# Performance work log

Measured on AMD Instinct MI355X. Metric: run time of the kernel, lower is better.

Reference implementation:

```python
import jax, jax.numpy as jnp
import numpy as np

N_HEAD = 16

def setup_inputs() -> dict:
    key = jax.random.key(0)
    k1, k2, k3 = jax.random.split(key, 3)
    B, T, C = 4, 2048, 1024
    x = jax.random.normal(k1, (B, T, C), dtype=jnp.float32)
    W_attn = jax.random.normal(k2, (C, 3 * C), dtype=jnp.float32) * (1.0 / np.sqrt(C))
    b_attn = jnp.zeros((3 * C,), dtype=jnp.float32)
    W_proj = jax.random.normal(k3, (C, C), dtype=jnp.float32) * (1.0 / np.sqrt(C))
    b_proj = jnp.zeros((C,), dtype=jnp.float32)
    return {"x": x, "W_attn": W_attn, "b_attn": b_attn, "W_proj": W_proj, "b_proj": b_proj, "train": 0}

def reference(x, W_attn, b_attn, W_proj, b_proj, train):
    # Causal self-attention, eval mode (dropout = identity since dropout=0.0 / train=False).
    B, T, C = x.shape
    H = N_HEAD
    hd = C // H
    qkv = x @ W_attn + b_attn                      # [B, T, 3C]
    q, k, v = jnp.split(qkv, 3, axis=-1)
    def to_heads(a):
        return a.reshape(B, T, H, hd).swapaxes(1, 2)   # [B, H, T, hd]
    q, k, v = to_heads(q), to_heads(k), to_heads(v)
    scale = 1.0 / jnp.sqrt(jnp.asarray(hd, dtype=x.dtype))
    attn = jnp.einsum('bhqd,bhkd->bhqk', q, k) * scale   # [B, H, T, T]
    causal = jnp.tril(jnp.ones((T, T), dtype=bool))
    attn = jnp.where(causal, attn, -jnp.inf)
    p = jax.nn.softmax(attn, axis=-1)
    y = jnp.einsum('bhqk,bhkd->bhqd', p, v)              # [B, H, T, hd]
    y = y.swapaxes(1, 2).reshape(B, T, C)
    return y @ W_proj + b_proj
```

## Files before the change

kernel.cpp:

```cpp
#include <hip/hip_runtime.h>
#include <hip/hip_bf16.h>
#include <math.h>

typedef __attribute__((ext_vector_type(8))) short short8;
typedef __attribute__((ext_vector_type(4))) short short4v;
typedef __attribute__((ext_vector_type(4))) float floatx4;
using bf16 = __hip_bfloat16;

#define DEVI __device__ __forceinline__

DEVI floatx4 fzero4() { floatx4 z; z[0]=0.f; z[1]=0.f; z[2]=0.f; z[3]=0.f; return z; }

DEVI float ex2(float x) {
  float r;
  asm("v_exp_f32 %0, %1" : "=v"(r) : "v"(x));
  return r;
}

DEVI unsigned short f2b(float x) {
  union { bf16 h; unsigned short u; } c;
  c.h = __float2bfloat16(x);
  return c.u;
}

DEVI floatx4 mfma16(short4v a, short4v b, floatx4 c) {
#if __has_builtin(__builtin_amdgcn_mfma_f32_16x16x16bf16_1k)
  return __builtin_amdgcn_mfma_f32_16x16x16bf16_1k(a, b, c, 0, 0, 0);
#else
  floatx4 d;
  asm("v_mfma_f32_16x16x16_bf16 %0, %1, %2, %3" : "=v"(d) : "v"(a), "v"(b), "v"(c));
  return d;
#endif
}

DEVI void gload16(const bf16* g, bf16* l) {
  typedef __attribute__((address_space(1))) const void gv_t;
  typedef __attribute__((address_space(3))) void lv_t;
  __builtin_amdgcn_global_load_lds((gv_t*)g, (lv_t*)l, 16, 0, 0);
}

__global__ __launch_bounds__(256) void k_cast(const float* __restrict__ in,
                                              bf16* __restrict__ out, int n) {
  int i = (blockIdx.x * 256 + threadIdx.x) * 8;
  if (i >= n) return;
  float4 a = *(const float4*)(in + i);
  float4 b = *(const float4*)(in + i + 4);
  short8 v;
  v[0] = (short)f2b(a.x); v[1] = (short)f2b(a.y);
  v[2] = (short)f2b(a.z); v[3] = (short)f2b(a.w);
  v[4] = (short)f2b(b.x); v[5] = (short)f2b(b.y);
  v[6] = (short)f2b(b.z); v[7] = (short)f2b(b.w);
  *(short8*)(out + i) = v;
}

__global__ __launch_bounds__(256) void k_transpose(const float* __restrict__ in,
                                                   bf16* __restrict__ out,
                                                   int R, int C) {
  __shared__ float tile[32][33];
  int x = blockIdx.x * 32 + threadIdx.x;
  for (int i = threadIdx.y; i < 32; i += 8) {
    int y = blockIdx.y * 32 + i;
    tile[i][threadIdx.x] = (y < R && x < C) ? in[(size_t)y * C + x] : 0.f;
  }
  __syncthreads();
  int ox = blockIdx.y * 32 + threadIdx.x;
  for (int i = threadIdx.y; i < 32; i += 8) {
    int oy = blockIdx.x * 32 + i;
    if (oy < C && ox < R) out[(size_t)oy * R + ox] = __float2bfloat16(tile[threadIdx.x][i]);
  }
}

template<int MODE>
__global__ __launch_bounds__(256) void k_gemm(
    const bf16* __restrict__ A, const bf16* __restrict__ Bt,
    const float* __restrict__ bias,
    bf16* __restrict__ Qo, bf16* __restrict__ Ko, bf16* __restrict__ Vo,
    float* __restrict__ Fo, int M, int N, int Kd) {
  __shared__ bf16 sA[128 * 32];
  __shared__ bf16 sB[128 * 32];
  const int tid = threadIdx.x;
  const int w = tid >> 6, l = tid & 63;
  const int lg = l >> 4, li = l & 15;
  const int wr = w >> 1, wc = w & 1;
  const int m0 = blockIdx.y * 128, n0 = blockIdx.x * 128;

  const int r0 = tid >> 2, ko0 = (tid & 3) * 8;
  const bf16* pa0 = A + (size_t)(m0 + r0) * Kd + ko0;
  const bf16* pa1 = A + (size_t)(m0 + 64 + r0) * Kd + ko0;
  const bf16* pb0 = Bt + (size_t)(n0 + r0) * Kd + ko0;
  const bf16* pb1 = Bt + (size_t)(n0 + 64 + r0) * Kd + ko0;

  floatx4 acc[4][4];
#pragma unroll
  for (int i = 0; i < 4; ++i)
#pragma unroll
    for (int j = 0; j < 4; ++j) acc[i][j] = fzero4();

  for (int k0 = 0; k0 < Kd; k0 += 32) {
    __syncthreads();
    gload16(pa0 + k0, sA + w * 512);
    gload16(pa1 + k0, sA + 2048 + w * 512);
    gload16(pb0 + k0, sB + w * 512);
    gload16(pb1 + k0, sB + 2048 + w * 512);
    __syncthreads();
    short8 af[4], bfr[4];
#pragma unroll
    for (int i = 0; i < 4; ++i)
      af[i] = *(const short8*)&sA[(wr * 64 + i * 16 + li) * 32 + lg * 8];
#pragma unroll
    for (int j = 0; j < 4; ++j)
      bfr[j] = *(const short8*)&sB[(wc * 64 + j * 16 + li) * 32 + lg * 8];
#pragma unroll
    for (int i = 0; i < 4; ++i)
#pragma unroll
      for (int j = 0; j < 4; ++j)
        acc[i][j] = __builtin_amdgcn_mfma_f32_16x16x32_bf16(af[i], bfr[j], acc[i][j], 0, 0, 0);
  }

#pragma unroll
  for (int i = 0; i < 4; ++i) {
#pragma unroll
    for (int j = 0; j < 4; ++j) {
      const int ng = n0 + wc * 64 + j * 16 + li;
      const float bs = bias[ng];
#pragma unroll
      for (int r = 0; r < 4; ++r) {
        const int mg = m0 + wr * 64 + i * 16 + lg * 4 + r;
        const float v = acc[i][j][r] + bs;
        if (MODE == 0) {
          const int bb = mg >> 11, t = mg & 2047;
          const int d = ng & 63;
          if (ng < 1024) {
            const int h = ng >> 6;
            Qo[(((size_t)bb * 16 + h) * 2048 + t) * 64 + d] = __float2bfloat16(v * 0.18033688011112042f);
          } else if (ng < 2048) {
            const int h = (ng - 1024) >> 6;
            Ko[(((size_t)bb * 16 + h) * 2048 + t) * 64 + d] = __float2bfloat16(v);
          } else {
            const int h = (ng - 2048) >> 6;
            Vo[(((size_t)bb * 16 + h) * 64 + d) * 2048 + t] = __float2bfloat16(v);
          }
        } else {
          Fo[(size_t)mg * N + ng] = v;
        }
      }
    }
  }
}

#define T_SEQ 2048

__global__ __launch_bounds__(256) void k_attn(
    const bf16* __restrict__ Q, const bf16* __restrict__ K,
    const bf16* __restrict__ Vt, bf16* __restrict__ Y) {
  __shared__ bf16 sK[2][64 * 64];
  __shared__ bf16 sV[2][64 * 64];

  const int tid = threadIdx.x;
  const int w = tid >> 6, l = tid & 63;
  const int lg = l >> 4, li = l & 15;
  const int bid = blockIdx.x;
  const int s = bid >> 3;
  const int bh = (bid & 7) * 8 + (s & 7);
  const int tb = 15 - (s >> 3);
  const int b = bh >> 4, h = bh & 15;

  const bf16* Qp = Q + (size_t)bh * (T_SEQ * 64);
  const bf16* Kp = K + (size_t)bh * (T_SEQ * 64);
  const bf16* Vp = Vt + (size_t)bh * (64 * T_SEQ);

  const int q0 = tb * 128;
  const int wq0 = q0 + w * 32;
  const int nst = (q0 + 128) >> 6;

  short8 aq[2][2];
#pragma unroll
  for (int rg = 0; rg < 2; ++rg)
#pragma unroll
    for (int dc = 0; dc < 2; ++dc)
      aq[rg][dc] = *(const short8*)(Qp + (size_t)(wq0 + rg * 16 + li) * 64 + dc * 32 + lg * 8);

  floatx4 o[2][4];
#pragma unroll
  for (int rg = 0; rg < 2; ++rg)
#pragma unroll
    for (int f = 0; f < 4; ++f) o[rg][f] = fzero4();
  float m[2] = {-INFINITY, -INFINITY};
  float lsum[2] = {0.f, 0.f};

  auto STAGE = [&](int buf, int k0) {
#pragma unroll
    for (int half = 0; half < 2; ++half) {
      const int c = half * 256 + tid;
      const int row = c >> 3, cs = c & 7;
      const int sc = cs ^ (row & 7);
      bf16* kb = &sK[buf][(half * 256 + w * 64) * 8];
      bf16* vb = &sV[buf][(half * 256 + w * 64) * 8];
      gload16(Kp + (size_t)(k0 + row) * 64 + sc * 8, kb);
      gload16(Vp + (size_t)row * T_SEQ + k0 + sc * 8, vb);
    }
  };

  int cur = 0;
  STAGE(0, 0);
  __syncthreads();
  for (int t = 0; t < nst; ++t) {
    const int k0 = t << 6;
    if (t + 1 < nst) STAGE(cur ^ 1, k0 + 64);
    if (k0 <= wq0 + 31) {
      floatx4 s[2][4];
#pragma unroll
      for (int kt = 0; kt < 4; ++kt) {
        const int rowk = kt * 16 + li;
        const short8 kb0 = *(const short8*)&sK[cur][rowk * 64 + ((lg ^ (rowk & 7)) * 8)];
        const short8 kb1 = *(const short8*)&sK[cur][rowk * 64 + (((4 + lg) ^ (rowk & 7)) * 8)];
#pragma unroll
        for (int rg = 0; rg < 2; ++rg) {
          floatx4 acc = __builtin_amdgcn_mfma_f32_16x16x32_bf16(kb0, aq[rg][0], fzero4(), 0, 0, 0);
          s[rg][kt] = __builtin_amdgcn_mfma_f32_16x16x32_bf16(kb1, aq[rg][1], acc, 0, 0, 0);
        }
      }
      if (k0 + 63 > wq0) {
#pragma unroll
        for (int rg = 0; rg < 2; ++rg) {
          const int qg = wq0 + rg * 16 + li;
#pragma unroll
          for (int kt = 0; kt < 4; ++kt) {
            const int kgb = k0 + kt * 16 + lg * 4;
#pragma unroll
            for (int r = 0; r < 4; ++r)
              if (kgb + r > qg) s[rg][kt][r] = -1e30f;
          }
        }
      }
      float pm[2];
#pragma unroll
      for (int rg = 0; rg < 2; ++rg) {
        float m0_ = fmaxf(fmaxf(s[rg][0][0], s[rg][0][1]), fmaxf(s[rg][0][2], s[rg][0][3]));
        float m1_ = fmaxf(fmaxf(s[rg][1][0], s[rg][1][1]), fmaxf(s[rg][1][2], s[rg][1][3]));
        float m2_ = fmaxf(fmaxf(s[rg][2][0], s[rg][2][1]), fmaxf(s[rg][2][2], s[rg][2][3]));
        float m3_ = fmaxf(fmaxf(s[rg][3][0], s[rg][3][1]), fmaxf(s[rg][3][2], s[rg][3][3]));
        float p = fmaxf(fmaxf(m0_, m1_), fmaxf(m2_, m3_));
        p = fmaxf(p, __shfl_xor(p, 16));
        p = fmaxf(p, __shfl_xor(p, 32));
        pm[rg] = p;
      }
      const float need = fmaxf(pm[0] - m[0], pm[1] - m[1]);
      if (!__all(need <= 8.0f)) {
#pragma unroll
        for (int rg = 0; rg < 2; ++rg) {
          const float mn = fmaxf(m[rg], pm[rg]);
          const float a = ex2(m[rg] - mn);
          m[rg] = mn;
          lsum[rg] *= a;
          float ar[4];
#pragma unroll
          for (int r = 0; r < 4; ++r) ar[r] = __shfl(a, lg * 4 + r);
#pragma unroll
          for (int f = 0; f < 4; ++f) {
            o[rg][f][0] *= ar[0]; o[rg][f][1] *= ar[1];
            o[rg][f][2] *= ar[2]; o[rg][f][3] *= ar[3];
          }
        }
      }
      short4v pa4[2][4];
#pragma unroll
      for (int rg = 0; rg < 2; ++rg) {
#pragma unroll
        for (int kt = 0; kt < 4; ++kt) {
          const float e0 = ex2(s[rg][kt][0] - m[rg]);
          const float e1 = ex2(s[rg][kt][1] - m[rg]);
          const float e2 = ex2(s[rg][kt][2] - m[rg]);
          const float e3 = ex2(s[rg][kt][3] - m[rg]);
          lsum[rg] += (e0 + e1) + (e2 + e3);
          short4v pv;
          pv[0] = (short)f2b(e0); pv[1] = (short)f2b(e1);
          pv[2] = (short)f2b(e2); pv[3] = (short)f2b(e3);
          pa4[rg][kt] = pv;
        }
      }
#pragma unroll
      for (int f = 0; f < 4; ++f) {
        const int rowv = f * 16 + li;
        const int rx = rowv & 7;
#pragma unroll
        for (int kt = 0; kt < 4; ++kt) {
          const int cc = 2 * kt + (lg >> 1);
          const short4v vb4 = *(const short4v*)&sV[cur][rowv * 64 + (((cc ^ rx) << 3) | ((lg & 1) << 2))];
          o[0][f] = mfma16(pa4[0][kt], vb4, o[0][f]);
          o[1][f] = mfma16(pa4[1][kt], vb4, o[1][f]);
        }
      }
    }
    __syncthreads();
    cur ^= 1;
  }
#pragma unroll
  for (int rg = 0; rg < 2; ++rg) {
    float Ls = lsum[rg];
    Ls += __shfl_xor(Ls, 16);
    Ls += __shfl_xor(Ls, 32);
#pragma unroll
    for (int r = 0; r < 4; ++r) {
      const float inv = 1.0f / __shfl(Ls, lg * 4 + r);
      const int qg = wq0 + rg * 16 + lg * 4 + r;
      const size_t base = ((size_t)b * T_SEQ + qg) * 1024 + h * 64;
#pragma unroll
      for (int f = 0; f < 4; ++f)
        Y[base + f * 16 + li] = __float2bfloat16(o[rg][f][r] * inv);
    }
  }
}

extern "C" void kernel_launch(void* const* d_in, const int* in_sizes, int n_in,
                              void* d_out, int out_size, void* d_ws, size_t ws_size,
                              hipStream_t stream) {
  const float* x      = (const float*)d_in[0];
  const float* W_attn = (const float*)d_in[1];
  const float* b_attn = (const float*)d_in[2];
  const float* W_proj = (const float*)d_in[3];
  const float* b_proj = (const float*)d_in[4];
  float* out = (float*)d_out;

  char* ws = (char*)d_ws;
  bf16* Wt_a = (bf16*)(ws);
  bf16* Wt_p = (bf16*)(ws + 6291456);
  bf16* Qb   = (bf16*)(ws + 8388608);
  bf16* Kb   = (bf16*)(ws + 25165824);
  bf16* Vtb  = (bf16*)(ws + 41943040);
  bf16* x_bf = (bf16*)(ws + 58720256);
  bf16* Yb   = x_bf;

  k_cast<<<4096, 256, 0, stream>>>(x, x_bf, 8388608);
  k_transpose<<<dim3(96, 32), dim3(32, 8), 0, stream>>>(W_attn, Wt_a, 1024, 3072);
  k_transpose<<<dim3(32, 32), dim3(32, 8), 0, stream>>>(W_proj, Wt_p, 1024, 1024);
  k_gemm<0><<<dim3(24, 64), 256, 0, stream>>>(x_bf, Wt_a, b_attn, Qb, Kb, Vtb,
                                              nullptr, 8192, 3072, 1024);
  k_attn<<<1024, 256, 0, stream>>>(Qb, Kb, Vtb, Yb);
  k_gemm<1><<<dim3(8, 64), 256, 0, stream>>>(Yb, Wt_p, b_proj, nullptr, nullptr,
                                             nullptr, out, 8192, 1024, 1024);
}
```

Measured before the change: 222.1 us.

## Double-buffer GEMM LDS tiles and remap blocks for XCD-local L2 reuse

Converts the GEMM k-loop to a two-stage LDS double buffer, issuing the next tile's global-to-LDS loads before computing the current one and waiting with vmcnt counts instead of full syncthreads. It also flattens the grid and remaps block indices so blocks dispatched to the same XCD work on neighbouring M rows, to improve L2 hit rates. The cost is doubled LDS per block, which could reduce occupancy, plus reliance on hand-written waitcnt correctness.

```diff
diff --git a/kernel.cpp b/kernel.cpp
--- a/kernel.cpp
+++ b/kernel.cpp
@@ -76,13 +76,15 @@
     const float* __restrict__ bias,
     bf16* __restrict__ Qo, bf16* __restrict__ Ko, bf16* __restrict__ Vo,
     float* __restrict__ Fo, int M, int N, int Kd) {
-  __shared__ bf16 sA[128 * 32];
-  __shared__ bf16 sB[128 * 32];
+  __shared__ bf16 sA[2][128 * 32];
+  __shared__ bf16 sB[2][128 * 32];
   const int tid = threadIdx.x;
   const int w = tid >> 6, l = tid & 63;
   const int lg = l >> 4, li = l & 15;
   const int wr = w >> 1, wc = w & 1;
-  const int m0 = blockIdx.y * 128, n0 = blockIdx.x * 128;
+  const int ii = blockIdx.x >> 3, xcd = blockIdx.x & 7;
+  const int bx = ii >> 3, by = xcd * 8 + (ii & 7);
+  const int m0 = by * 128, n0 = bx * 128;
 
   const int r0 = tid >> 2, ko0 = (tid & 3) * 8;
   const bf16* pa0 = A + (size_t)(m0 + r0) * Kd + ko0;
@@ -96,25 +98,37 @@
 #pragma unroll
     for (int j = 0; j < 4; ++j) acc[i][j] = fzero4();
 
+  auto STAGE = [&](int buf, int k0) {
+    gload16(pa0 + k0, &sA[buf][w * 512]);
+    gload16(pa1 + k0, &sA[buf][2048 + w * 512]);
+    gload16(pb0 + k0, &sB[buf][w * 512]);
+    gload16(pb1 + k0, &sB[buf][2048 + w * 512]);
+  };
+
+  STAGE(0, 0);
+  int cur = 0;
   for (int k0 = 0; k0 < Kd; k0 += 32) {
-    __syncthreads();
-    gload16(pa0 + k0, sA + w * 512);
-    gload16(pa1 + k0, sA + 2048 + w * 512);
-    gload16(pb0 + k0, sB + w * 512);
-    gload16(pb1 + k0, sB + 2048 + w * 512);
-    __syncthreads();
+    if (k0 + 32 < Kd) {
+      STAGE(cur ^ 1, k0 + 32);
+      asm volatile("s_waitcnt vmcnt(4)" ::: "memory");
+    } else {
+      asm volatile("s_waitcnt vmcnt(0)" ::: "memory");
+    }
+    __builtin_amdgcn_s_barrier();
     short8 af[4], bfr[4];
 #pragma unroll
     for (int i = 0; i < 4; ++i)
-      af[i] = *(const short8*)&sA[(wr * 64 + i * 16 + li) * 32 + lg * 8];
+      af[i] = *(const short8*)&sA[cur][(wr * 64 + i * 16 + li) * 32 + lg * 8];
 #pragma unroll
     for (int j = 0; j < 4; ++j)
-      bfr[j] = *(const short8*)&sB[(wc * 64 + j * 16 + li) * 32 + lg * 8];
+      bfr[j] = *(const short8*)&sB[cur][(wc * 64 + j * 16 + li) * 32 + lg * 8];
 #pragma unroll
     for (int i = 0; i < 4; ++i)
 #pragma unroll
       for (int j = 0; j < 4; ++j)
         acc[i][j] = __builtin_amdgcn_mfma_f32_16x16x32_bf16(af[i], bfr[j], acc[i][j], 0, 0, 0);
+    __builtin_amdgcn_s_barrier();
+    cur ^= 1;
   }
 
 #pragma unroll
@@ -334,9 +348,9 @@
   k_cast<<<4096, 256, 0, stream>>>(x, x_bf, 8388608);
   k_transpose<<<dim3(96, 32), dim3(32, 8), 0, stream>>>(W_attn, Wt_a, 1024, 3072);
   k_transpose<<<dim3(32, 32), dim3(32, 8), 0, stream>>>(W_proj, Wt_p, 1024, 1024);
-  k_gemm<0><<<dim3(24, 64), 256, 0, stream>>>(x_bf, Wt_a, b_attn, Qb, Kb, Vtb,
-                                              nullptr, 8192, 3072, 1024);
+  k_gemm<0><<<1536, 256, 0, stream>>>(x_bf, Wt_a, b_attn, Qb, Kb, Vtb,
+                                      nullptr, 8192, 3072, 1024);
   k_attn<<<1024, 256, 0, stream>>>(Qb, Kb, Vtb, Yb);
-  k_gemm<1><<<dim3(8, 64), 256, 0, stream>>>(Yb, Wt_p, b_proj, nullptr, nullptr,
-                                             nullptr, out, 8192, 1024, 1024);
-}
+  k_gemm<1><<<512, 256, 0, stream>>>(Yb, Wt_p, b_proj, nullptr, nullptr,
+                                     nullptr, out, 8192, 1024, 1024);
+}
```

Measured after the change: 199.9 us. 1.11x faster.
